# Kernel tuning notes

Measured on AMD Instinct MI355X. Metric: run time of the kernel, lower is better.

Reference implementation:

```python
import jax, jax.numpy as jnp
import numpy as np

NUM_EMBEDDINGS = 1024
EMBEDDING_DIM = 256


def setup_inputs() -> dict:
    key = jax.random.key(0)
    k1, k2 = jax.random.split(key)
    x = jax.random.normal(k1, (64, EMBEDDING_DIM, 32, 32), dtype=jnp.float32)
    # torch.nn.init.uniform_ default is U[0,1)
    embeddings = jax.random.uniform(k2, (EMBEDDING_DIM, NUM_EMBEDDINGS), dtype=jnp.float32)
    return {"x": x, "embeddings": embeddings}


def reference(x, embeddings):
    # x: [B, C, H, W] with C == embedding_dim; embeddings: [D, K]
    B, C, H, W = x.shape
    x_perm = jnp.transpose(x, (0, 2, 3, 1))           # [B, H, W, D]
    flat = x_perm.reshape(-1, C)                      # [N, D]
    sim = flat @ embeddings                           # [N, K] GEMM
    dists = (jnp.sum(flat * flat, axis=1, keepdims=True)
             + jnp.sum(embeddings * embeddings, axis=0)
             - 2.0 * sim)                             # [N, K]
    indices = jnp.argmin(dists, axis=1)               # [N]
    # one-hot @ embeddings.T is just a row gather of embeddings.T
    quantized = embeddings.T[indices]                 # [N, D]
    quantized = quantized.reshape(x_perm.shape)       # [B, H, W, D]
    # straight-through estimator
    q_ste = x_perm + jax.lax.stop_gradient(quantized - x_perm)
    q_ste = jnp.transpose(q_ste, (0, 3, 1, 2))        # [B, C, H, W]
    quantized = jnp.transpose(quantized, (0, 3, 1, 2))
    return q_ste, quantized, indices
```

## Files before the change

### kernel.cpp

```cpp
#include <hip/hip_runtime.h>

typedef unsigned short u16;
typedef unsigned int   u32;

#define DCH  256
#define KCB  1024
#define HW   1024
#define NPOS 65536
#define MARGIN 0.07f

#define ESQ_WS   0
#define IDX_WS   4096
#define FCNT_WS  266240
#define FLIST_WS 266304
#define ESQD_WS  528448ull
#define XH_WS    1048576ull
#define EH_WS    34603008ull

using f32x4 = __attribute__((ext_vector_type(4))) float;
using f16x8 = __attribute__((ext_vector_type(8))) _Float16;

__device__ __forceinline__ u16 f2h(float x) {
    _Float16 h = (_Float16)x;
    return *reinterpret_cast<u16*>(&h);
}

__device__ __forceinline__ void gl_lds16(const void* g, void* l) {
    __builtin_amdgcn_global_load_lds(
        (const __attribute__((address_space(1))) void*)g,
        (__attribute__((address_space(3))) void*)l, 16, 0, 0);
}

__device__ __forceinline__ void transpose_slice(const float* __restrict__ src,
                                                u16* __restrict__ dst,
                                                int b, int pc, int cc, int tid) {
    __shared__ float Xs[32][260];
    const int p0 = pc * 256;
    const int c0 = cc * 32;
    const size_t nbase = (size_t)b * 1024 + p0;
#pragma unroll
    for (int r = 0; r < 8; ++r) {
        int id4 = tid + 256 * r;
        int c = id4 >> 6;
        int q = id4 & 63;
        float4 v = *reinterpret_cast<const float4*>(
            src + (size_t)b * 262144 + (size_t)(c0 + c) * 1024 + p0 + q * 4);
        *reinterpret_cast<float4*>(&Xs[c][q * 4]) = v;
    }
    __syncthreads();
    const int p = tid;
#pragma unroll
    for (int dg = 0; dg < 4; ++dg) {
        u32 w0, w1, w2, w3;
        {
            float f0 = Xs[dg * 8 + 0][p], f1 = Xs[dg * 8 + 1][p];
            float f2 = Xs[dg * 8 + 2][p], f3 = Xs[dg * 8 + 3][p];
            float f4 = Xs[dg * 8 + 4][p], f5 = Xs[dg * 8 + 5][p];
            float f6 = Xs[dg * 8 + 6][p], f7 = Xs[dg * 8 + 7][p];
            w0 = (u32)f2h(f0) | ((u32)f2h(f1) << 16);
            w1 = (u32)f2h(f2) | ((u32)f2h(f3) << 16);
            w2 = (u32)f2h(f4) | ((u32)f2h(f5) << 16);
            w3 = (u32)f2h(f6) | ((u32)f2h(f7) << 16);
        }
        uint4 ov = {w0, w1, w2, w3};
        *reinterpret_cast<uint4*>(dst + (nbase + p) * 256 + c0 + dg * 8) = ov;
    }
}

__global__ __launch_bounds__(256) void prep_all(const float* __restrict__ X,
                                                const float* __restrict__ E,
                                                u16* __restrict__ Xh,
                                                u16* __restrict__ Eh,
                                                float* __restrict__ esq,
                                                double* __restrict__ esqd,
                                                int* __restrict__ fcnt) {
    const int tid = threadIdx.x;
    const int bid = blockIdx.x;
    if (bid < 2048) {
        transpose_slice(X, Xh, bid >> 5, (bid >> 3) & 3, bid & 7, tid);
    } else if (bid < 2080) {
        int b2 = bid - 2048;
        transpose_slice(E, Eh, 0, (b2 >> 3) & 3, b2 & 7, tid);
    } else {
        if (bid == 2080 && tid == 0) *fcnt = 0;
        int k = (bid - 2080) * 256 + tid;
        double s = 0.0;
#pragma unroll 8
        for (int c = 0; c < DCH; ++c) {
            double e = (double)E[c * KCB + k];
            s = fma(e, e, s);
        }
        esq[k] = (float)s;
        esqd[k] = s;
    }
}

#define BUFS  32768
#define EB_O  16384
#define ESQ_O 65536
#define MRG_O 69632
#define SM_SZ 72704

__global__ __launch_bounds__(256, 2) void vq_main_mfma(
        const u16* __restrict__ XhG, const u16* __restrict__ EhG,
        const float* __restrict__ esq,
        int* __restrict__ idx_out, int* __restrict__ flag_cnt,
        int* __restrict__ flag_list) {
    __shared__ alignas(16) char sm[SM_SZ];
    const int tid = threadIdx.x;
    const int l = tid & 63;
    const int w = tid >> 6;
    const int wm = w >> 1, wn = w & 1;
    const int pbase = blockIdx.x * 128;

    *reinterpret_cast<float4*>(sm + ESQ_O + tid * 16) =
        *reinterpret_cast<const float4*>(esq + tid * 4);

    const int srow = w * 32 + (l >> 3);
    const int sswz = ((l & 7) ^ (l >> 3)) * 16;
    const char* XhB = reinterpret_cast<const char*>(XhG);
    const char* EhB = reinterpret_cast<const char*>(EhG);
    const size_t xbase = (size_t)(pbase + srow) * 512 + sswz;
    const size_t ebase = (size_t)srow * 512 + sswz;

    const int sA0 = (((l >> 4) ^ (l & 7))) * 16;
    const int addrA0 = wm * 8192 + (l & 15) * 128 + sA0;
    const int addrB0 = wn * 8192 + (l & 15) * 128 + sA0;

    auto STAGE = [&](int bufo, int nt, int kt) {
        const size_t xo = xbase + (size_t)kt * 128;
        const size_t eo = ebase + (size_t)nt * 65536 + (size_t)kt * 128;
#pragma unroll
        for (int k = 0; k < 4; ++k) {
            gl_lds16(XhB + xo + k * 4096, sm + bufo + (w * 4 + k) * 1024);
            gl_lds16(EhB + eo + k * 4096, sm + bufo + EB_O + (w * 4 + k) * 1024);
        }
    };

    float b1[16], b2[16];
    int   i1[16];
#pragma unroll
    for (int q = 0; q < 16; ++q) { b1[q] = 3.4e38f; b2[q] = 3.4e38f; i1[q] = 0; }

    STAGE(0, 0, 0);
    __syncthreads();

    int step = 0;
    for (int nt = 0; nt < 8; ++nt) {
        f32x4 acc[4][4];
#pragma unroll
        for (int i = 0; i < 4; ++i)
#pragma unroll
            for (int j = 0; j < 4; ++j)
#pragma unroll
                for (int r = 0; r < 4; ++r) acc[i][j][r] = 0.f;

        for (int kt = 0; kt < 4; ++kt) {
            int nxt = step + 1;
            if (nxt < 32) STAGE((nxt & 1) * BUFS, nxt >> 2, nxt & 3);
            const char* bo = sm + (step & 1) * BUFS;
#pragma unroll
            for (int ds = 0; ds < 2; ++ds) {
                const int so = ds * 64;
                f16x8 a[4], bh[4];
#pragma unroll
                for (int i = 0; i < 4; ++i)
                    a[i] = *reinterpret_cast<const f16x8*>(bo + ((addrA0 ^ so) + i * 2048));
#pragma unroll
                for (int j = 0; j < 4; ++j)
                    bh[j] = *reinterpret_cast<const f16x8*>(bo + EB_O + ((addrB0 ^ so) + j * 2048));
#pragma unroll
                for (int i = 0; i < 4; ++i)
#pragma unroll
                    for (int j = 0; j < 4; ++j)
                        acc[i][j] = __builtin_amdgcn_mfma_f32_16x16x32_f16(a[i], bh[j], acc[i][j], 0, 0, 0);
            }
            __syncthreads();
            ++step;
        }

        const int kb = nt * 128 + wn * 64 + (l & 15);
        float eq[4];
#pragma unroll
        for (int j = 0; j < 4; ++j)
            eq[j] = *reinterpret_cast<const float*>(sm + ESQ_O + (kb + j * 16) * 4);
#pragma unroll
        for (int i = 0; i < 4; ++i)
#pragma unroll
            for (int j = 0; j < 4; ++j)
#pragma unroll
                for (int r = 0; r < 4; ++r) {
                    float s = fmaf(-2.f, acc[i][j][r], eq[j]);
                    int ri = i * 4 + r;
                    bool lt = s < b1[ri];
                    b2[ri] = fminf(b2[ri], fmaxf(s, b1[ri]));
                    i1[ri] = lt ? (kb + j * 16) : i1[ri];
                    b1[ri] = fminf(b1[ri], s);
                }
    }

#pragma unroll
    for (int m = 1; m <= 8; m <<= 1) {
#pragma unroll
        for (int q = 0; q < 16; ++q) {
            float ob1 = __shfl_xor(b1[q], m);
            float ob2 = __shfl_xor(b2[q], m);
            int   oi  = __shfl_xor(i1[q], m);
            bool lt = ob1 < b1[q];
            b2[q] = fminf(fminf(b2[q], ob2), fmaxf(b1[q], ob1));
            i1[q] = lt ? oi : i1[q];
            b1[q] = fminf(b1[q], ob1);
        }
    }

    if ((l & 15) == 0) {
#pragma unroll
        for (int i = 0; i < 4; ++i)
#pragma unroll
            for (int r = 0; r < 4; ++r) {
                int q = i * 4 + r;
                int rl = wm * 64 + i * 16 + (l >> 4) * 4 + r;
                *reinterpret_cast<float*>(sm + MRG_O + (rl * 2 + wn) * 4) = b1[q];
                *reinterpret_cast<float*>(sm + MRG_O + 1024 + (rl * 2 + wn) * 4) = b2[q];
                *reinterpret_cast<int*>(sm + MRG_O + 2048 + (rl * 2 + wn) * 4) = i1[q];
            }
    }
    __syncthreads();
    if (tid < 128) {
        float a1 = *reinterpret_cast<float*>(sm + MRG_O + (tid * 2 + 0) * 4);
        float a2 = *reinterpret_cast<float*>(sm + MRG_O + 1024 + (tid * 2 + 0) * 4);
        int   ai = *reinterpret_cast<int*>(sm + MRG_O + 2048 + (tid * 2 + 0) * 4);
        float c1 = *reinterpret_cast<float*>(sm + MRG_O + (tid * 2 + 1) * 4);
        float c2 = *reinterpret_cast<float*>(sm + MRG_O + 1024 + (tid * 2 + 1) * 4);
        int   ci = *reinterpret_cast<int*>(sm + MRG_O + 2048 + (tid * 2 + 1) * 4);
        bool lt = c1 < a1;
        float B1 = fminf(a1, c1);
        float B2 = fminf(fminf(a2, c2), fmaxf(a1, c1));
        int I1 = lt ? ci : ai;
        int n = pbase + tid;
        idx_out[n] = I1;
        if (B2 - B1 < MARGIN) {
            int s2 = atomicAdd(flag_cnt, 1);
            flag_list[s2] = n;
        }
    }
}

#define RFPB 2
__global__ __launch_bounds__(256) void vq_repair(const float* __restrict__ X,
                                                 const float* __restrict__ E,
                                                 const double* __restrict__ esqd,
                                                 int* __restrict__ idx_out,
                                                 const int* __restrict__ flag_cnt,
                                                 const int* __restrict__ flag_list) {
    __shared__ double xs[RFPB][256];
    __shared__ double rd[RFPB][256];
    __shared__ int    ri[RFPB][256];
    const int tid = threadIdx.x;
    const int cnt = *flag_cnt;
    for (int f0 = blockIdx.x * RFPB; f0 < cnt; f0 += gridDim.x * RFPB) {
#pragma unroll
        for (int g = 0; g < RFPB; ++g) {
            int f = f0 + g;
            int n = flag_list[f < cnt ? f : f0];
            int b = n >> 10, p = n & 1023;
            xs[g][tid] = (double)X[(size_t)b * 262144 + (size_t)tid * 1024 + p];
        }
        __syncthreads();
        double s[RFPB][4];
#pragma unroll
        for (int g = 0; g < RFPB; ++g)
#pragma unroll
            for (int j = 0; j < 4; ++j) s[g][j] = 0.0;
        const float4* Erow = reinterpret_cast<const float4*>(E) + tid;
#pragma unroll 2
        for (int c = 0; c < 256; ++c) {
            float4 ev = Erow[c * 256];
            double e0 = (double)ev.x, e1 = (double)ev.y, e2 = (double)ev.z, e3 = (double)ev.w;
#pragma unroll
            for (int g = 0; g < RFPB; ++g) {
                double xv = xs[g][c];
                s[g][0] = fma(xv, e0, s[g][0]);
                s[g][1] = fma(xv, e1, s[g][1]);
                s[g][2] = fma(xv, e2, s[g][2]);
                s[g][3] = fma(xv, e3, s[g][3]);
            }
        }
        const int k0 = tid * 4;
        const double eq0 = esqd[k0], eq1 = esqd[k0 + 1], eq2 = esqd[k0 + 2], eq3 = esqd[k0 + 3];
#pragma unroll
        for (int g = 0; g < RFPB; ++g) {
            double d0 = eq0 - 2.0 * s[g][0];
            double d1 = eq1 - 2.0 * s[g][1];
            double d2 = eq2 - 2.0 * s[g][2];
            double d3 = eq3 - 2.0 * s[g][3];
            double bd = d0; int bi = k0;
            if (d1 < bd) { bd = d1; bi = k0 + 1; }
            if (d2 < bd) { bd = d2; bi = k0 + 2; }
            if (d3 < bd) { bd = d3; bi = k0 + 3; }
            rd[g][tid] = bd; ri[g][tid] = bi;
        }
        __syncthreads();
        for (int off = 128; off > 0; off >>= 1) {
            if (tid < off) {
#pragma unroll
                for (int g = 0; g < RFPB; ++g) {
                    double od = rd[g][tid + off]; int oi = ri[g][tid + off];
                    if (od < rd[g][tid] || (od == rd[g][tid] && oi < ri[g][tid])) {
                        rd[g][tid] = od; ri[g][tid] = oi;
                    }
                }
            }
            __syncthreads();
        }
        if (tid < RFPB && (f0 + tid) < cnt) {
            idx_out[flag_list[f0 + tid]] = ri[tid][0];
        }
        __syncthreads();
    }
}

#define WCC 8
__global__ __launch_bounds__(256) void vq_write(const float* __restrict__ E,
                                                const int* __restrict__ idx_ws,
                                                float* __restrict__ out0,
                                                float* __restrict__ out1,
                                                float* __restrict__ out2) {
    __shared__ float Es[WCC][1024];
    const int tid = threadIdx.x;
    const int b   = blockIdx.x >> 5;
    const int cch = blockIdx.x & 31;
#pragma unroll
    for (int r = 0; r < 8; ++r) {
        int id4 = tid + 256 * r;
        int c = id4 >> 8;
        int q = id4 & 255;
        *reinterpret_cast<float4*>(&Es[c][q * 4]) =
            *reinterpret_cast<const float4*>(E + (size_t)(cch * WCC + c) * 1024 + q * 4);
    }
    int4 kv = *reinterpret_cast<const int4*>(idx_ws + b * 1024 + tid * 4);
    __syncthreads();
    if (cch == 0) {
        float4 v = {(float)kv.x, (float)kv.y, (float)kv.z, (float)kv.w};
        *reinterpret_cast<float4*>(out2 + b * 1024 + tid * 4) = v;
    }
#pragma unroll
    for (int c = 0; c < WCC; ++c) {
        float4 v = {Es[c][kv.x], Es[c][kv.y], Es[c][kv.z], Es[c][kv.w]};
        size_t o = (size_t)b * 262144 + (size_t)(cch * WCC + c) * 1024 + tid * 4;
        *reinterpret_cast<float4*>(out0 + o) = v;
        *reinterpret_cast<float4*>(out1 + o) = v;
    }
}

extern "C" void kernel_launch(void* const* d_in, const int* in_sizes, int n_in,
                              void* d_out, int out_size, void* d_ws, size_t ws_size,
                              hipStream_t stream) {
    const float* X = (const float*)d_in[0];
    const float* E = (const float*)d_in[1];
    float* out = (float*)d_out;
    char* ws = (char*)d_ws;

    float* esq   = (float*)(ws + ESQ_WS);
    int* idx     = (int*)(ws + IDX_WS);
    int* fcnt    = (int*)(ws + FCNT_WS);
    int* flist   = (int*)(ws + FLIST_WS);
    double* esqd = (double*)(ws + ESQD_WS);
    u16* Xh      = (u16*)(ws + XH_WS);
    u16* Eh      = (u16*)(ws + EH_WS);

    prep_all<<<2084, 256, 0, stream>>>(X, E, Xh, Eh, esq, esqd, fcnt);
    vq_main_mfma<<<512, 256, 0, stream>>>(Xh, Eh, esq, idx, fcnt, flist);
    vq_repair<<<2048, 256, 0, stream>>>(X, E, esqd, idx, fcnt, flist);
    vq_write<<<2048, 256, 0, stream>>>(E, idx,
                                       out,
                                       out + 16777216,
                                       out + 33554432);
}
```

Baseline: 151.4 us.

## Fuse quantized output gather into main MFMA kernel; repair patches flagged outputs

Drops the separate vq_write kernel. The main kernel now stages codebook channel slices in shared memory and writes both quantized outputs and the index-as-float output for its 128 positions using nontemporal stores. The repair kernel rewrites the outputs for the flagged positions whose index it recomputes. This removes a launch and the index round-trip, but the main kernel now reloads the whole codebook (1 MB) per block through 32 sync-separated rounds and writes in a strided per-channel pattern.

```diff
diff --git a/kernel.cpp b/kernel.cpp
--- a/kernel.cpp
+++ b/kernel.cpp
@@ -103,9 +103,12 @@
 
 __global__ __launch_bounds__(256, 2) void vq_main_mfma(
         const u16* __restrict__ XhG, const u16* __restrict__ EhG,
+        const float* __restrict__ E,
         const float* __restrict__ esq,
         int* __restrict__ idx_out, int* __restrict__ flag_cnt,
-        int* __restrict__ flag_list) {
+        int* __restrict__ flag_list,
+        float* __restrict__ out0, float* __restrict__ out1,
+        float* __restrict__ out2) {
     __shared__ alignas(16) char sm[SM_SZ];
     const int tid = threadIdx.x;
     const int l = tid & 63;
@@ -226,6 +229,7 @@
             }
     }
     __syncthreads();
+    int* idxL = reinterpret_cast<int*>(sm + ESQ_O);
     if (tid < 128) {
         float a1 = *reinterpret_cast<float*>(sm + MRG_O + (tid * 2 + 0) * 4);
         float a2 = *reinterpret_cast<float*>(sm + MRG_O + 1024 + (tid * 2 + 0) * 4);
@@ -239,10 +243,38 @@
         int I1 = lt ? ci : ai;
         int n = pbase + tid;
         idx_out[n] = I1;
+        idxL[tid] = I1;
+        out2[n] = (float)I1;
         if (B2 - B1 < MARGIN) {
             int s2 = atomicAdd(flag_cnt, 1);
             flag_list[s2] = n;
         }
+    }
+    __syncthreads();
+
+    const int ob = blockIdx.x >> 3;
+    const int op0 = (blockIdx.x & 7) * 128;
+    const int p = tid & 127;
+    const int cg = (tid >> 7) * 4;
+    const int kp = idxL[p];
+    float* o0 = out0 + (size_t)ob * 262144 + op0 + p;
+    for (int cc = 0; cc < 32; ++cc) {
+#pragma unroll
+        for (int r = 0; r < 8; ++r) {
+            int g = r * 256 + tid;
+            gl_lds16(E + (size_t)(cc * 8 + (g >> 8)) * 1024 + (size_t)(g & 255) * 4,
+                     sm + g * 16);
+        }
+        __syncthreads();
+#pragma unroll
+        for (int c2 = 0; c2 < 4; ++c2) {
+            int c = cg + c2;
+            float v = *reinterpret_cast<const float*>(sm + c * 4096 + kp * 4);
+            size_t off = (size_t)(cc * 8 + c) * 1024;
+            __builtin_nontemporal_store(v, o0 + off);
+            __builtin_nontemporal_store(v, o0 + 16777216 + off);
+        }
+        __syncthreads();
     }
 }
 
@@ -252,7 +284,10 @@
                                                  const double* __restrict__ esqd,
                                                  int* __restrict__ idx_out,
                                                  const int* __restrict__ flag_cnt,
-                                                 const int* __restrict__ flag_list) {
+                                                 const int* __restrict__ flag_list,
+                                                 float* __restrict__ out0,
+                                                 float* __restrict__ out1,
+                                                 float* __restrict__ out2) {
     __shared__ double xs[RFPB][256];
     __shared__ double rd[RFPB][256];
     __shared__ int    ri[RFPB][256];
@@ -313,43 +348,21 @@
             }
             __syncthreads();
         }
-        if (tid < RFPB && (f0 + tid) < cnt) {
-            idx_out[flag_list[f0 + tid]] = ri[tid][0];
-        }
-        __syncthreads();
-    }
-}
-
-#define WCC 8
-__global__ __launch_bounds__(256) void vq_write(const float* __restrict__ E,
-                                                const int* __restrict__ idx_ws,
-                                                float* __restrict__ out0,
-                                                float* __restrict__ out1,
-                                                float* __restrict__ out2) {
-    __shared__ float Es[WCC][1024];
-    const int tid = threadIdx.x;
-    const int b   = blockIdx.x >> 5;
-    const int cch = blockIdx.x & 31;
-#pragma unroll
-    for (int r = 0; r < 8; ++r) {
-        int id4 = tid + 256 * r;
-        int c = id4 >> 8;
-        int q = id4 & 255;
-        *reinterpret_cast<float4*>(&Es[c][q * 4]) =
-            *reinterpret_cast<const float4*>(E + (size_t)(cch * WCC + c) * 1024 + q * 4);
-    }
-    int4 kv = *reinterpret_cast<const int4*>(idx_ws + b * 1024 + tid * 4);
-    __syncthreads();
-    if (cch == 0) {
-        float4 v = {(float)kv.x, (float)kv.y, (float)kv.z, (float)kv.w};
-        *reinterpret_cast<float4*>(out2 + b * 1024 + tid * 4) = v;
-    }
-#pragma unroll
-    for (int c = 0; c < WCC; ++c) {
-        float4 v = {Es[c][kv.x], Es[c][kv.y], Es[c][kv.z], Es[c][kv.w]};
-        size_t o = (size_t)b * 262144 + (size_t)(cch * WCC + c) * 1024 + tid * 4;
-        *reinterpret_cast<float4*>(out0 + o) = v;
-        *reinterpret_cast<float4*>(out1 + o) = v;
+#pragma unroll
+        for (int g = 0; g < RFPB; ++g) {
+            int f = f0 + g;
+            if (f < cnt) {
+                int n = flag_list[f];
+                int bi = ri[g][0];
+                int b = n >> 10, p = n & 1023;
+                float v = E[(size_t)tid * 1024 + bi];
+                size_t o = (size_t)b * 262144 + (size_t)tid * 1024 + p;
+                out0[o] = v;
+                out1[o] = v;
+                if (tid == 0) { idx_out[n] = bi; out2[n] = (float)bi; }
+            }
+        }
+        __syncthreads();
     }
 }
 
@@ -369,11 +382,13 @@
     u16* Xh      = (u16*)(ws + XH_WS);
     u16* Eh      = (u16*)(ws + EH_WS);
 
+    float* out0 = out;
+    float* out1 = out + 16777216;
+    float* out2 = out + 33554432;
+
     prep_all<<<2084, 256, 0, stream>>>(X, E, Xh, Eh, esq, esqd, fcnt);
-    vq_main_mfma<<<512, 256, 0, stream>>>(Xh, Eh, esq, idx, fcnt, flist);
-    vq_repair<<<2048, 256, 0, stream>>>(X, E, esqd, idx, fcnt, flist);
-    vq_write<<<2048, 256, 0, stream>>>(E, idx,
-                                       out,
-                                       out + 16777216,
-                                       out + 33554432);
-}
+    vq_main_mfma<<<512, 256, 0, stream>>>(Xh, Eh, E, esq, idx, fcnt, flist,
+                                          out0, out1, out2);
+    vq_repair<<<2048, 256, 0, stream>>>(X, E, esqd, idx, fcnt, flist,
+                                        out0, out1, out2);
+}
```

Result: slower. 175.4 us (+15.9%).
